# Kernel optimization log

Hardware: AMD Instinct MI355X
Metric: run time of the kernel (lower is better)

Reference implementation:

```python
import jax, jax.numpy as jnp
import numpy as np

HIDDEN = 512
LATENT = 256
NUM_NODE_TYPES = 16


def setup_inputs() -> dict:
    key = jax.random.key(0)
    ks = jax.random.split(key, 9)
    s = lambda fan_in: 1.0 / np.sqrt(fan_in)
    return {
        "z": jax.random.normal(ks[0], (1024, LATENT), dtype=jnp.float32),
        "num_nodes": 128,
        "W_z": jax.random.uniform(ks[1], (LATENT, HIDDEN), jnp.float32, -s(LATENT), s(LATENT)),
        "b_z": jax.random.uniform(ks[2], (HIDDEN,), jnp.float32, -s(LATENT), s(LATENT)),
        "W_node": jax.random.uniform(ks[3], (HIDDEN, NUM_NODE_TYPES), jnp.float32, -s(HIDDEN), s(HIDDEN)),
        "b_node": jax.random.uniform(ks[4], (NUM_NODE_TYPES,), jnp.float32, -s(HIDDEN), s(HIDDEN)),
        "W_e1": jax.random.uniform(ks[5], (2 * HIDDEN, HIDDEN), jnp.float32, -s(2 * HIDDEN), s(2 * HIDDEN)),
        "b_e1": jax.random.uniform(ks[6], (HIDDEN,), jnp.float32, -s(2 * HIDDEN), s(2 * HIDDEN)),
        "W_e2": jax.random.uniform(ks[7], (HIDDEN, 1), jnp.float32, -s(HIDDEN), s(HIDDEN)),
        "b_e2": jax.random.uniform(ks[8], (1,), jnp.float32, -s(HIDDEN), s(HIDDEN)),
    }


def reference(z, num_nodes, W_z, b_z, W_node, b_node, W_e1, b_e1, W_e2, b_e2):
    # h: [B, H]
    h = jax.nn.relu(z @ W_z + b_z)
    B = z.shape[0]
    # h_expanded: [B, N, H] (same h replicated per node, as in the original)
    h_expanded = jnp.broadcast_to(h[:, None, :], (B, num_nodes, h.shape[-1]))
    node_logits = h_expanded @ W_node + b_node  # [B, N, T]
    # Every (i, j) pair in the original loop uses cat(h, h) -> identical scalar per batch.
    h_pair = jnp.concatenate([h, h], axis=-1)  # [B, 2H]
    p = jax.nn.sigmoid(jax.nn.relu(h_pair @ W_e1 + b_e1) @ W_e2 + b_e2)  # [B, 1]
    # Scatter onto strict lower triangle (j < i), zeros elsewhere.
    tril = jnp.tril(jnp.ones((num_nodes, num_nodes), dtype=z.dtype), k=-1)  # [N, N]
    edge_probs = p[:, :, None] * tril[None, :, :]  # [B, N, N]
    return node_logits, edge_probs
```

## Files before the change

kernel.cpp:

```cpp
#include <hip/hip_runtime.h>
#include <hip/hip_bf16.h>
#include <math.h>

#define BB 1024
#define LL 256
#define HH 512
#define TT 16
#define NN 128

#define NODE_F4 (BB * NN * TT / 4)
#define EDGE_F4 (BB * NN * NN / 4)

typedef short bf16x8 __attribute__((ext_vector_type(8)));
typedef float f32x4  __attribute__((ext_vector_type(4)));

static __device__ __forceinline__ short bfbits(float f) {
    __hip_bfloat16 h = __float2bfloat16(f);
    return *reinterpret_cast<short*>(&h);
}

static __device__ __forceinline__ int h_addr(int row, int col) {
    return (row << 10) + ((((col >> 3) ^ (row & 7)) << 4)) + ((col & 7) << 1);
}

__device__ __forceinline__ void transpose_tile(const float* __restrict__ in,
                                               __hip_bfloat16* __restrict__ out,
                                               int k0, int n0, int Kdim, bool fold,
                                               __hip_bfloat16 (*tile)[34]) {
    const int tx = threadIdx.x & 31;
    const int ty = threadIdx.x >> 5;
    #pragma unroll
    for (int r = ty; r < 32; r += 8) {
        float v = in[(k0 + r) * HH + n0 + tx];
        if (fold) v += in[(k0 + r + HH) * HH + n0 + tx];
        tile[r][tx] = __float2bfloat16(v);
    }
    __syncthreads();
    #pragma unroll
    for (int r = ty; r < 32; r += 8) {
        out[(n0 + r) * Kdim + k0 + tx] = tile[tx][r];
    }
}

__global__ __launch_bounds__(256) void k_prep(const float* __restrict__ Wz,
                                              const float* __restrict__ We1,
                                              const float* __restrict__ Wn,
                                              __hip_bfloat16* __restrict__ WzT,
                                              __hip_bfloat16* __restrict__ WsumT,
                                              __hip_bfloat16* __restrict__ WnT,
                                              float* __restrict__ p_acc) {
    __shared__ __hip_bfloat16 tile[32][34];
    const int bid = blockIdx.x;
    const int tid = threadIdx.x;
    if (bid < 128) {
        transpose_tile(Wz, WzT, (bid >> 4) * 32, (bid & 15) * 32, LL, false, tile);
    } else if (bid < 384) {
        const int t = bid - 128;
        transpose_tile(We1, WsumT, (t >> 4) * 32, (t & 15) * 32, HH, true, tile);
    } else if (bid < 416) {
        const int u = (bid - 384) * 256 + tid;
        WnT[u] = __float2bfloat16(Wn[(u & 511) * TT + (u >> 9)]);
    } else if (tid < 256) {
        ((float4*)p_acc)[tid] = make_float4(0.f, 0.f, 0.f, 0.f);
    }
}

__global__ __launch_bounds__(512) void k_fused(const float* __restrict__ z,
                                               const __hip_bfloat16* __restrict__ WzT,
                                               const __hip_bfloat16* __restrict__ WsumT,
                                               const __hip_bfloat16* __restrict__ WnT,
                                               const float* __restrict__ bz,
                                               const float* __restrict__ be1,
                                               const float* __restrict__ We2,
                                               const float* __restrict__ bn,
                                               float* __restrict__ p_acc,
                                               float4* __restrict__ out) {
    __shared__ char  hbuf[16384];
    __shared__ f32x4 nod_lds[8][64];
    __shared__ float pw_lds[8][16];
    __shared__ float nodef[16][16];

    const int tid  = threadIdx.x;
    const int w    = tid >> 6;
    const int lane = tid & 63;
    const int l16  = lane & 15, quad = lane >> 4;
    const int g = blockIdx.x >> 2, q = blockIdx.x & 3;
    const int r0 = g << 4;

    {
        bf16x8 afr[8];
        const float4* zf = (const float4*)(z + (r0 + l16) * LL);
        #pragma unroll
        for (int kt = 0; kt < 8; ++kt) {
            float4 v0 = zf[quad * 2 + kt * 8];
            float4 v1 = zf[quad * 2 + kt * 8 + 1];
            bf16x8 a;
            a[0] = bfbits(v0.x); a[1] = bfbits(v0.y); a[2] = bfbits(v0.z); a[3] = bfbits(v0.w);
            a[4] = bfbits(v1.x); a[5] = bfbits(v1.y); a[6] = bfbits(v1.z); a[7] = bfbits(v1.w);
            afr[kt] = a;
        }
        #pragma unroll
        for (int i = 0; i < 4; ++i) {
            const int nt = (w << 2) + i;
            const short* Bp = (const short*)WzT + (nt * 16 + l16) * LL + quad * 8;
            f32x4 acc = {0.f, 0.f, 0.f, 0.f};
            #pragma unroll
            for (int kt = 0; kt < 8; ++kt) {
                bf16x8 b = *(const bf16x8*)(Bp + kt * 32);
                acc = __builtin_amdgcn_mfma_f32_16x16x32_bf16(afr[kt], b, acc, 0, 0, 0);
            }
            const int col = nt * 16 + l16;
            const float bb = bz[col];
            #pragma unroll
            for (int r = 0; r < 4; ++r) {
                float hv = fmaxf(acc[r] + bb, 0.f);
                *(short*)(hbuf + h_addr(quad * 4 + r, col)) = bfbits(hv);
            }
        }
    }
    __syncthreads();

    {
        f32x4 acc = {0.f, 0.f, 0.f, 0.f};
        const short* Bp = (const short*)WnT + l16 * HH + quad * 8;
        #pragma unroll
        for (int kk = 0; kk < 2; ++kk) {
            const int kt = w * 2 + kk;
            bf16x8 a = *(const bf16x8*)(hbuf + h_addr(l16, quad * 8 + kt * 32));
            bf16x8 b = *(const bf16x8*)(Bp + kt * 32);
            acc = __builtin_amdgcn_mfma_f32_16x16x32_bf16(a, b, acc, 0, 0, 0);
        }
        nod_lds[w][lane] = acc;
    }

    {
        const int nt = q * 8 + w;
        const short* Bp = (const short*)WsumT + (nt * 16 + l16) * HH + quad * 8;
        f32x4 acc = {0.f, 0.f, 0.f, 0.f};
        #pragma unroll
        for (int kt = 0; kt < 16; ++kt) {
            bf16x8 a = *(const bf16x8*)(hbuf + h_addr(l16, quad * 8 + kt * 32));
            bf16x8 b = *(const bf16x8*)(Bp + kt * 32);
            acc = __builtin_amdgcn_mfma_f32_16x16x32_bf16(a, b, acc, 0, 0, 0);
        }
        const int col = nt * 16 + l16;
        const float bb = be1[col], w2 = We2[col];
        float sr[4];
        #pragma unroll
        for (int r = 0; r < 4; ++r) sr[r] = fmaxf(acc[r] + bb, 0.f) * w2;
        #pragma unroll
        for (int off = 1; off < 16; off <<= 1) {
            #pragma unroll
            for (int r = 0; r < 4; ++r) sr[r] += __shfl_xor(sr[r], off);
        }
        if (l16 == 0) {
            #pragma unroll
            for (int r = 0; r < 4; ++r) pw_lds[w][quad * 4 + r] = sr[r];
        }
    }
    __syncthreads();

    if (w == 0) {
        f32x4 s = nod_lds[0][lane];
        #pragma unroll
        for (int ww = 1; ww < 8; ++ww) {
            f32x4 t = nod_lds[ww][lane];
            s[0] += t[0]; s[1] += t[1]; s[2] += t[2]; s[3] += t[3];
        }
        const float bb = bn[l16];
        #pragma unroll
        for (int r = 0; r < 4; ++r)
            nodef[quad * 4 + r][l16] = s[r] + bb;
    }
    if (w == 1 && lane < 16) {
        float t = 0.f;
        #pragma unroll
        for (int ww = 0; ww < 8; ++ww) t += pw_lds[ww][lane];
        atomicAdd(p_acc + r0 + lane, t);
    }
    __syncthreads();

    {
        const float4* nf4 = (const float4*)nodef;
        #pragma unroll
        for (int i = 0; i < 4; ++i) {
            const int idx = i * 512 + tid;
            const int bl  = idx >> 7;
            const int rem = idx & 127;
            const int nl  = rem >> 2;
            const int t4  = rem & 3;
            out[(r0 + bl) * 512 + (q * 32 + nl) * 4 + t4] = nf4[bl * 4 + t4];
        }
    }
}

__global__ __launch_bounds__(256) void k_edge(const float* __restrict__ p_acc,
                                              const float* __restrict__ be2,
                                              f32x4* __restrict__ oedge) {
    const int gid = blockIdx.x * 256 + threadIdx.x;
    const float b2 = be2[0];
    #pragma unroll
    for (int it = 0; it < 8; ++it) {
        const int e  = it * (2048 * 256) + gid;
        const int b  = e >> 12;
        const int i  = (e >> 5) & 127;
        const int j0 = (e & 31) << 2;
        const float pv = 1.f / (1.f + expf(-(p_acc[b] + b2)));
        f32x4 v;
        v[0] = (j0 + 0 < i) ? pv : 0.f;
        v[1] = (j0 + 1 < i) ? pv : 0.f;
        v[2] = (j0 + 2 < i) ? pv : 0.f;
        v[3] = (j0 + 3 < i) ? pv : 0.f;
        __builtin_nontemporal_store(v, oedge + e);
    }
}

extern "C" void kernel_launch(void* const* d_in, const int* in_sizes, int n_in,
                              void* d_out, int out_size, void* d_ws, size_t ws_size,
                              hipStream_t stream) {
    const float* z    = (const float*)d_in[0];
    const float* Wz   = (const float*)d_in[2];
    const float* bz   = (const float*)d_in[3];
    const float* Wn   = (const float*)d_in[4];
    const float* bn   = (const float*)d_in[5];
    const float* We1  = (const float*)d_in[6];
    const float* be1  = (const float*)d_in[7];
    const float* We2  = (const float*)d_in[8];
    const float* be2  = (const float*)d_in[9];
    float* out = (float*)d_out;

    char* base = (char*)d_ws;
    __hip_bfloat16* WzT    = (__hip_bfloat16*)(base);
    __hip_bfloat16* WsumT  = (__hip_bfloat16*)(base +  256 * 1024);
    __hip_bfloat16* WnT    = (__hip_bfloat16*)(base +  768 * 1024);
    float*          p_acc  = (float*)(base + 784 * 1024);

    k_prep<<<417, 256, 0, stream>>>(Wz, We1, Wn, WzT, WsumT, WnT, p_acc);

    k_fused<<<256, 512, 0, stream>>>(z, WzT, WsumT, WnT,
                                     bz, be1, We2, bn, p_acc, (float4*)out);

    k_edge<<<2048, 256, 0, stream>>>(p_acc, be2, (f32x4*)((float4*)out + NODE_F4));

    (void)in_sizes; (void)n_in; (void)out_size; (void)ws_size;
}
```

Measured before the change: 127.0 us.

## Fuse edge-probability kernel into main kernel and compute full hidden sum per block

```diff
diff --git a/kernel.cpp b/kernel.cpp
--- a/kernel.cpp
+++ b/kernel.cpp
@@ -47,8 +47,7 @@
                                               const float* __restrict__ Wn,
                                               __hip_bfloat16* __restrict__ WzT,
                                               __hip_bfloat16* __restrict__ WsumT,
-                                              __hip_bfloat16* __restrict__ WnT,
-                                              float* __restrict__ p_acc) {
+                                              __hip_bfloat16* __restrict__ WnT) {
     __shared__ __hip_bfloat16 tile[32][34];
     const int bid = blockIdx.x;
     const int tid = threadIdx.x;
@@ -57,28 +56,27 @@
     } else if (bid < 384) {
         const int t = bid - 128;
         transpose_tile(We1, WsumT, (t >> 4) * 32, (t & 15) * 32, HH, true, tile);
-    } else if (bid < 416) {
+    } else {
         const int u = (bid - 384) * 256 + tid;
         WnT[u] = __float2bfloat16(Wn[(u & 511) * TT + (u >> 9)]);
-    } else if (tid < 256) {
-        ((float4*)p_acc)[tid] = make_float4(0.f, 0.f, 0.f, 0.f);
-    }
-}
-
-__global__ __launch_bounds__(512) void k_fused(const float* __restrict__ z,
-                                               const __hip_bfloat16* __restrict__ WzT,
-                                               const __hip_bfloat16* __restrict__ WsumT,
-                                               const __hip_bfloat16* __restrict__ WnT,
-                                               const float* __restrict__ bz,
-                                               const float* __restrict__ be1,
-                                               const float* __restrict__ We2,
-                                               const float* __restrict__ bn,
-                                               float* __restrict__ p_acc,
-                                               float4* __restrict__ out) {
+    }
+}
+
+__global__ __launch_bounds__(512) void k_mega(const float* __restrict__ z,
+                                              const __hip_bfloat16* __restrict__ WzT,
+                                              const __hip_bfloat16* __restrict__ WsumT,
+                                              const __hip_bfloat16* __restrict__ WnT,
+                                              const float* __restrict__ bz,
+                                              const float* __restrict__ be1,
+                                              const float* __restrict__ We2,
+                                              const float* __restrict__ bn,
+                                              const float* __restrict__ be2,
+                                              f32x4* __restrict__ out) {
     __shared__ char  hbuf[16384];
     __shared__ f32x4 nod_lds[8][64];
     __shared__ float pw_lds[8][16];
     __shared__ float nodef[16][16];
+    __shared__ float pfin[16];
 
     const int tid  = threadIdx.x;
     const int w    = tid >> 6;
@@ -134,28 +132,39 @@
     }
 
     {
-        const int nt = q * 8 + w;
-        const short* Bp = (const short*)WsumT + (nt * 16 + l16) * HH + quad * 8;
-        f32x4 acc = {0.f, 0.f, 0.f, 0.f};
+        f32x4 acc[4];
+        #pragma unroll
+        for (int i = 0; i < 4; ++i) acc[i] = (f32x4){0.f, 0.f, 0.f, 0.f};
         #pragma unroll
         for (int kt = 0; kt < 16; ++kt) {
             bf16x8 a = *(const bf16x8*)(hbuf + h_addr(l16, quad * 8 + kt * 32));
-            bf16x8 b = *(const bf16x8*)(Bp + kt * 32);
-            acc = __builtin_amdgcn_mfma_f32_16x16x32_bf16(a, b, acc, 0, 0, 0);
-        }
-        const int col = nt * 16 + l16;
-        const float bb = be1[col], w2 = We2[col];
-        float sr[4];
-        #pragma unroll
-        for (int r = 0; r < 4; ++r) sr[r] = fmaxf(acc[r] + bb, 0.f) * w2;
-        #pragma unroll
-        for (int off = 1; off < 16; off <<= 1) {
-            #pragma unroll
-            for (int r = 0; r < 4; ++r) sr[r] += __shfl_xor(sr[r], off);
+            #pragma unroll
+            for (int i = 0; i < 4; ++i) {
+                const int nt = (w << 2) + i;
+                bf16x8 b = *(const bf16x8*)((const short*)WsumT +
+                            (nt * 16 + l16) * HH + quad * 8 + kt * 32);
+                acc[i] = __builtin_amdgcn_mfma_f32_16x16x32_bf16(a, b, acc[i], 0, 0, 0);
+            }
+        }
+        float psum[4] = {0.f, 0.f, 0.f, 0.f};
+        #pragma unroll
+        for (int i = 0; i < 4; ++i) {
+            const int col = ((w << 2) + i) * 16 + l16;
+            const float bb = be1[col], w2 = We2[col];
+            float sr[4];
+            #pragma unroll
+            for (int r = 0; r < 4; ++r) sr[r] = fmaxf(acc[i][r] + bb, 0.f) * w2;
+            #pragma unroll
+            for (int off = 1; off < 16; off <<= 1) {
+                #pragma unroll
+                for (int r = 0; r < 4; ++r) sr[r] += __shfl_xor(sr[r], off);
+            }
+            #pragma unroll
+            for (int r = 0; r < 4; ++r) psum[r] += sr[r];
         }
         if (l16 == 0) {
             #pragma unroll
-            for (int r = 0; r < 4; ++r) pw_lds[w][quad * 4 + r] = sr[r];
+            for (int r = 0; r < 4; ++r) pw_lds[w][quad * 4 + r] = psum[r];
         }
     }
     __syncthreads();
@@ -176,12 +185,12 @@
         float t = 0.f;
         #pragma unroll
         for (int ww = 0; ww < 8; ++ww) t += pw_lds[ww][lane];
-        atomicAdd(p_acc + r0 + lane, t);
-    }
-    __syncthreads();
-
-    {
-        const float4* nf4 = (const float4*)nodef;
+        pfin[lane] = 1.f / (1.f + expf(-(t + be2[0])));
+    }
+    __syncthreads();
+
+    {
+        const f32x4* nf4 = (const f32x4*)nodef;
         #pragma unroll
         for (int i = 0; i < 4; ++i) {
             const int idx = i * 512 + tid;
@@ -189,29 +198,30 @@
             const int rem = idx & 127;
             const int nl  = rem >> 2;
             const int t4  = rem & 3;
-            out[(r0 + bl) * 512 + (q * 32 + nl) * 4 + t4] = nf4[bl * 4 + t4];
-        }
-    }
-}
-
-__global__ __launch_bounds__(256) void k_edge(const float* __restrict__ p_acc,
-                                              const float* __restrict__ be2,
-                                              f32x4* __restrict__ oedge) {
-    const int gid = blockIdx.x * 256 + threadIdx.x;
-    const float b2 = be2[0];
-    #pragma unroll
-    for (int it = 0; it < 8; ++it) {
-        const int e  = it * (2048 * 256) + gid;
-        const int b  = e >> 12;
-        const int i  = (e >> 5) & 127;
-        const int j0 = (e & 31) << 2;
-        const float pv = 1.f / (1.f + expf(-(p_acc[b] + b2)));
-        f32x4 v;
-        v[0] = (j0 + 0 < i) ? pv : 0.f;
-        v[1] = (j0 + 1 < i) ? pv : 0.f;
-        v[2] = (j0 + 2 < i) ? pv : 0.f;
-        v[3] = (j0 + 3 < i) ? pv : 0.f;
-        __builtin_nontemporal_store(v, oedge + e);
+            __builtin_nontemporal_store(nf4[bl * 4 + t4],
+                out + (r0 + bl) * 512 + (q * 32 + nl) * 4 + t4);
+        }
+    }
+
+    {
+        f32x4* oedge = out + NODE_F4;
+        #pragma unroll
+        for (int i = 0; i < 4; ++i) {
+            const int b = r0 + (q << 2) + i;
+            const float pv = pfin[(q << 2) + i];
+            #pragma unroll
+            for (int it = 0; it < 8; ++it) {
+                const int e  = it * 512 + tid;
+                const int ii = e >> 5;
+                const int j0 = (e & 31) << 2;
+                f32x4 v;
+                v[0] = (j0 + 0 < ii) ? pv : 0.f;
+                v[1] = (j0 + 1 < ii) ? pv : 0.f;
+                v[2] = (j0 + 2 < ii) ? pv : 0.f;
+                v[3] = (j0 + 3 < ii) ? pv : 0.f;
+                __builtin_nontemporal_store(v, oedge + b * 4096 + e);
+            }
+        }
     }
 }
 
@@ -233,14 +243,11 @@
     __hip_bfloat16* WzT    = (__hip_bfloat16*)(base);
     __hip_bfloat16* WsumT  = (__hip_bfloat16*)(base +  256 * 1024);
     __hip_bfloat16* WnT    = (__hip_bfloat16*)(base +  768 * 1024);
-    float*          p_acc  = (float*)(base + 784 * 1024);
-
-    k_prep<<<417, 256, 0, stream>>>(Wz, We1, Wn, WzT, WsumT, WnT, p_acc);
-
-    k_fused<<<256, 512, 0, stream>>>(z, WzT, WsumT, WnT,
-                                     bz, be1, We2, bn, p_acc, (float4*)out);
-
-    k_edge<<<2048, 256, 0, stream>>>(p_acc, be2, (f32x4*)((float4*)out + NODE_F4));
+
+    k_prep<<<416, 256, 0, stream>>>(Wz, We1, Wn, WzT, WsumT, WnT);
+
+    k_mega<<<256, 512, 0, stream>>>(z, WzT, WsumT, WnT,
+                                    bz, be1, We2, bn, be2, (f32x4*)out);
 
     (void)in_sizes; (void)n_in; (void)out_size; (void)ws_size;
 }
```

After: 134.3 us. 1.06x slower.
